# Kernel optimization log

Measured on AMD Instinct MI355X. Metric: run time of the kernel, lower is better.

The kernel has to match this reference:

```python
import jax, jax.numpy as jnp
import numpy as np

EPS = 1e-10

def norm_t(x, axis):
    # zero-mean + L2 normalize along `axis` (standard NCC normalization)
    xc = x - jnp.mean(x, axis=axis, keepdims=True)
    return xc / (jnp.linalg.norm(xc, axis=axis, keepdims=True) + EPS)

def setup_inputs() -> dict:
    key = jax.random.key(0)
    k1, k2 = jax.random.split(key)
    input_compressed = jax.random.normal(k1, (1, 16, 131072), dtype=jnp.float32)  # [B, K, N]
    cmat = jax.random.normal(k2, (16, 1024), dtype=jnp.float32)                   # [K, D]
    return {"input_compressed": input_compressed, "cmat": cmat}

def reference(input_compressed, cmat):
    a = norm_t(input_compressed, axis=-2)          # [B, K, N], normalized over K
    b = norm_t(cmat, axis=0)                       # [K, D],    normalized over K
    ncc = jnp.einsum('bkn,kd->bnd', a, b)          # [B, N, D] correlation volume
    # torch: argmax(transpose(ncc,-2,-1), dim=-2) -> argmax over D -> [B, N]
    pred_depths = jnp.argmax(ncc, axis=-1)         # [B, N] int depth-bin indices
    return pred_depths
```

## Files before the change

kernel.cpp:

```cpp
#include <hip/hip_runtime.h>
#include <hip/hip_bf16.h>
#include <math.h>

#define N_PTS  131072
#define K_DIM  16
#define D_BINS 1024
#define MARGIN_P 6e-4f

typedef short bf16x8 __attribute__((ext_vector_type(8)));
typedef float f32x4  __attribute__((ext_vector_type(4)));

#define WS_OFF_BN  64
#define WS_OFF_B1  65600
#define WS_OFF_B2  98368
#define WS_OFF_Z   131136
#define WS_OFF_WL  131152
#define WS_NEED    655440

__device__ __forceinline__ void norm_np(const float* __restrict__ p,
                                        int stride, int n, float* __restrict__ a) {
#pragma clang fp contract(off)
    float v[K_DIM];
#pragma unroll
    for (int k = 0; k < K_DIM; ++k) v[k] = p[(size_t)k * stride + n];
    float s = v[0];
#pragma unroll
    for (int k = 1; k < K_DIM; ++k) s = s + v[k];
    const float mean = s / 16.0f;
    float sq[K_DIM];
#pragma unroll
    for (int k = 0; k < K_DIM; ++k) { a[k] = v[k] - mean; sq[k] = a[k] * a[k]; }
    float ss = sq[0];
#pragma unroll
    for (int k = 1; k < K_DIM; ++k) ss = ss + sq[k];
    const float denom = sqrtf(ss) + 1e-10f;
#pragma unroll
    for (int k = 0; k < K_DIM; ++k) a[k] = a[k] / denom;
}

__device__ __forceinline__ unsigned short bf16_bits(float f) {
    __hip_bfloat16 h = __float2bfloat16(f);
    unsigned short u;
    __builtin_memcpy(&u, &h, 2);
    return u;
}
__device__ __forceinline__ float bf16_val(float f) {
    return __bfloat162float(__float2bfloat16(f));
}

__global__ __launch_bounds__(256) void prep_b(
    const float* __restrict__ cmat, float* __restrict__ bnT,
    unsigned short* __restrict__ B1, unsigned short* __restrict__ B2,
    unsigned short* __restrict__ zblk, int* __restrict__ wl_count) {
#pragma clang fp contract(off)
    if (blockIdx.x == 0) {
        if (threadIdx.x == 0) *wl_count = 0;
        if (threadIdx.x < 8) zblk[threadIdx.x] = 0;
    }
    const int d = blockIdx.x * 256 + threadIdx.x;
    if (d >= D_BINS) return;

    float t[K_DIM];
    norm_np(cmat, D_BINS, d, t);

    const int tile = d >> 4, n = d & 15;
#pragma unroll
    for (int k = 0; k < K_DIM; ++k) {
        bnT[d * K_DIM + k] = t[k];
        const float hi_f = bf16_val(t[k]);
        const int idx = tile * 256 + ((k >> 3) * 16 + n) * 8 + (k & 7);
        B1[idx] = bf16_bits(t[k]);
        B2[idx] = bf16_bits(t[k] - hi_f);
    }
}

__global__ __launch_bounds__(512, 8) void mfma_screen(
    const float* __restrict__ x, const uint4* __restrict__ B1,
    const uint4* __restrict__ B2,
    int* __restrict__ out, int* __restrict__ wl, int* __restrict__ wl_count) {
#pragma clang fp contract(off)
    __shared__ uint4 ldsB[2048];

    {
#pragma unroll
        for (int j = 0; j < 4; ++j)
            ldsB[threadIdx.x + j * 512] = B1[threadIdx.x + j * 512];
    }

    const int lane = threadIdx.x & 63;
    const int wv   = threadIdx.x >> 6;
    const int W    = blockIdx.x * 8 + wv;
    const int P    = W * 16;
    const int m    = lane & 15;
    const int q    = lane >> 4;

    bf16x8 A;
    {
        float a[K_DIM];
        norm_np(x, N_PTS, P + m, a);
        unsigned short els[8];
#pragma unroll
        for (int j = 0; j < 8; ++j) {
            const int k = (q & 1) * 8 + j;
            if (q < 2) els[j] = bf16_bits(a[k]);
            else       els[j] = bf16_bits(a[k] - bf16_val(a[k]));
        }
        __builtin_memcpy(&A, els, 16);
    }

    __syncthreads();

    const uint4* b1p = ldsB + (lane & 31);
    const int b2base = (lane < 32) ? lane : 2048;
    const int b2step = (lane < 32) ? 32 : 0;

    unsigned ub1[4], ub2[4];
#pragma unroll
    for (int r = 0; r < 4; ++r) { ub1[r] = 0u; ub2[r] = 0u; }

    const unsigned mask  = 0xFFFFF800u;
    const unsigned dbase = 2047u - (unsigned)m;

#pragma unroll 4
    for (int i = 0; i < 64; ++i) {
        const uint4 w1 = b1p[i * 32];
        const uint4 w2 = B2[b2base + i * b2step];
        const bf16x8 bf1 = __builtin_bit_cast(bf16x8, w1);
        const bf16x8 bf2 = __builtin_bit_cast(bf16x8, w2);

        f32x4 acc = __builtin_amdgcn_mfma_f32_16x16x32_bf16(
            A, bf1, (f32x4){2.f, 2.f, 2.f, 2.f}, 0, 0, 0);
        acc = __builtin_amdgcn_mfma_f32_16x16x32_bf16(A, bf2, acc, 0, 0, 0);

        const unsigned dcomp = dbase - (unsigned)(i * 16);
#pragma unroll
        for (int r = 0; r < 4; ++r) {
            const unsigned u = (__float_as_uint(acc[r]) & mask) | dcomp;
            const unsigned nx = max(ub1[r], u);
            ub2[r] = max(ub2[r], min(ub1[r], u));
            ub1[r] = nx;
        }
    }

#pragma unroll
    for (int r = 0; r < 4; ++r) {
        unsigned u1 = ub1[r], u2 = ub2[r];
#pragma unroll
        for (int s = 1; s <= 8; s <<= 1) {
            const unsigned o1 = (unsigned)__shfl_xor((int)u1, s, 16);
            const unsigned o2 = (unsigned)__shfl_xor((int)u2, s, 16);
            const unsigned n1 = max(u1, o1);
            u2 = max(min(u1, o1), max(u2, o2));
            u1 = n1;
        }
        if (m == 0) {
            const int p  = P + q * 4 + r;
            const float s1 = __uint_as_float(u1 & mask);
            const float s2 = __uint_as_float(u2 & mask);
            if (s1 - s2 > MARGIN_P) {
                out[p] = 2047 - (int)(u1 & 2047u);
            } else {
                const int pos = atomicAdd(wl_count, 1);
                wl[pos] = p;
            }
        }
    }
}

__global__ __launch_bounds__(256) void ncc_exact_refine(
    const float* __restrict__ x, const float* __restrict__ bnT,
    int* __restrict__ out, const int* __restrict__ wl,
    const int* __restrict__ wl_count) {
#pragma clang fp contract(off)
    const int count  = *wl_count;
    const int lane   = threadIdx.x & 63;
    const int wave   = (blockIdx.x * 256 + threadIdx.x) >> 6;
    const int nwaves = (gridDim.x * 256) >> 6;

    for (int i = wave; i < count; i += nwaves) {
        const int n = wl[i];
        float a[K_DIM];
        norm_np(x, N_PTS, n, a);

        float best = -3.402823466e38f;
        int   idx  = 0x7fffffff;
        const float4* b4 = (const float4*)bnT;
        for (int t = 0; t < 16; ++t) {
            const int d = t * 64 + lane;
            const float4 q0 = b4[d * 4 + 0];
            const float4 q1 = b4[d * 4 + 1];
            const float4 q2 = b4[d * 4 + 2];
            const float4 q3 = b4[d * 4 + 3];
            float sc;
            sc = a[0] * q0.x;
            sc = sc + a[1]  * q0.y; sc = sc + a[2]  * q0.z; sc = sc + a[3]  * q0.w;
            sc = sc + a[4]  * q1.x; sc = sc + a[5]  * q1.y; sc = sc + a[6]  * q1.z;
            sc = sc + a[7]  * q1.w; sc = sc + a[8]  * q2.x; sc = sc + a[9]  * q2.y;
            sc = sc + a[10] * q2.z; sc = sc + a[11] * q2.w; sc = sc + a[12] * q3.x;
            sc = sc + a[13] * q3.y; sc = sc + a[14] * q3.z; sc = sc + a[15] * q3.w;
            if (sc > best) { best = sc; idx = d; }
        }
#pragma unroll
        for (int mk = 1; mk <= 32; mk <<= 1) {
            const float ob = __shfl_xor(best, mk);
            const int   oi = __shfl_xor(idx,  mk);
            if (ob > best || (ob == best && oi < idx)) { best = ob; idx = oi; }
        }
        if (lane == 0) out[n] = idx;
    }
}

__global__ __launch_bounds__(256) void ncc_argmax_np32(
    const float* __restrict__ x, const float* __restrict__ bnT,
    int* __restrict__ out) {
#pragma clang fp contract(off)
    const int n = blockIdx.x * 256 + threadIdx.x;
    float a[K_DIM];
    norm_np(x, N_PTS, n, a);

    float best = -3.402823466e38f;
    int   idx  = 0;
    const float4* b4 = (const float4*)bnT;
#pragma unroll 2
    for (int d = 0; d < D_BINS; ++d) {
        const float4 q0 = b4[d * 4 + 0];
        const float4 q1 = b4[d * 4 + 1];
        const float4 q2 = b4[d * 4 + 2];
        const float4 q3 = b4[d * 4 + 3];
        float sc;
        sc = a[0] * q0.x;
        sc = sc + a[1]  * q0.y; sc = sc + a[2]  * q0.z; sc = sc + a[3]  * q0.w;
        sc = sc + a[4]  * q1.x; sc = sc + a[5]  * q1.y; sc = sc + a[6]  * q1.z;
        sc = sc + a[7]  * q1.w; sc = sc + a[8]  * q2.x; sc = sc + a[9]  * q2.y;
        sc = sc + a[10] * q2.z; sc = sc + a[11] * q2.w; sc = sc + a[12] * q3.x;
        sc = sc + a[13] * q3.y; sc = sc + a[14] * q3.z; sc = sc + a[15] * q3.w;
        if (sc > best) { best = sc; idx = d; }
    }
    out[n] = idx;
}

__global__ __launch_bounds__(256) void normalize_rows_only(
    const float* __restrict__ cmat, float* __restrict__ bnT) {
#pragma clang fp contract(off)
    const int d = blockIdx.x * 256 + threadIdx.x;
    if (d >= D_BINS) return;
    float t[K_DIM];
    norm_np(cmat, D_BINS, d, t);
#pragma unroll
    for (int k = 0; k < K_DIM; ++k) bnT[d * K_DIM + k] = t[k];
}

extern "C" void kernel_launch(void* const* d_in, const int* in_sizes, int n_in,
                              void* d_out, int out_size, void* d_ws, size_t ws_size,
                              hipStream_t stream) {
    const float* x    = (const float*)d_in[0];
    const float* cmat = (const float*)d_in[1];
    int* out = (int*)d_out;
    char* ws = (char*)d_ws;

    if (ws_size >= (size_t)WS_NEED) {
        int*            wl_count = (int*)ws;
        float*          bnT      = (float*)(ws + WS_OFF_BN);
        unsigned short* B1       = (unsigned short*)(ws + WS_OFF_B1);
        unsigned short* B2       = (unsigned short*)(ws + WS_OFF_B2);
        unsigned short* zblk     = (unsigned short*)(ws + WS_OFF_Z);
        int*            wl       = (int*)(ws + WS_OFF_WL);

        prep_b<<<4, 256, 0, stream>>>(cmat, bnT, B1, B2, zblk, wl_count);
        mfma_screen<<<1024, 512, 0, stream>>>(
            x, (const uint4*)(ws + WS_OFF_B1), (const uint4*)(ws + WS_OFF_B2),
            out, wl, wl_count);
        ncc_exact_refine<<<512, 256, 0, stream>>>(x, bnT, out, wl, wl_count);
    } else {
        float* bnT = (float*)(ws + WS_OFF_BN);
        normalize_rows_only<<<4, 256, 0, stream>>>(cmat, bnT);
        ncc_argmax_np32<<<512, 256, 0, stream>>>(x, bnT, out);
    }
}
```

Before: 106.9 us.

## Screen with single fp16 MFMA instead of split-bf16 pair, widen margin

Replaces the two-pass split-bf16 screening (hi and lo parts of A and B) with a single fp16 MFMA per tile. The B-low array and its global reads are dropped, and the A-low half is zeroed. The candidate margin is raised to cover the larger fp16 error, and the exact refine kernel gets twice as many blocks. This halves MFMA and global B traffic in the screening loop, but the wider margin may send more points to the exact refine pass.

```diff
diff --git a/kernel.cpp b/kernel.cpp
--- a/kernel.cpp
+++ b/kernel.cpp
@@ -1,21 +1,19 @@
 #include <hip/hip_runtime.h>
-#include <hip/hip_bf16.h>
+#include <hip/hip_fp16.h>
 #include <math.h>
 
 #define N_PTS  131072
 #define K_DIM  16
 #define D_BINS 1024
-#define MARGIN_P 6e-4f
-
-typedef short bf16x8 __attribute__((ext_vector_type(8)));
-typedef float f32x4  __attribute__((ext_vector_type(4)));
+#define MARGIN_P 3.2e-3f
+
+typedef _Float16 f16x8 __attribute__((ext_vector_type(8)));
+typedef float    f32x4 __attribute__((ext_vector_type(4)));
 
 #define WS_OFF_BN  64
-#define WS_OFF_B1  65600
-#define WS_OFF_B2  98368
-#define WS_OFF_Z   131136
-#define WS_OFF_WL  131152
-#define WS_NEED    655440
+#define WS_OFF_BH  65600
+#define WS_OFF_WL  98368
+#define WS_NEED    (WS_OFF_WL + 4 * N_PTS)
 
 __device__ __forceinline__ void norm_np(const float* __restrict__ p,
                                         int stride, int n, float* __restrict__ a) {
@@ -38,25 +36,16 @@
     for (int k = 0; k < K_DIM; ++k) a[k] = a[k] / denom;
 }
 
-__device__ __forceinline__ unsigned short bf16_bits(float f) {
-    __hip_bfloat16 h = __float2bfloat16(f);
-    unsigned short u;
-    __builtin_memcpy(&u, &h, 2);
-    return u;
-}
-__device__ __forceinline__ float bf16_val(float f) {
-    return __bfloat162float(__float2bfloat16(f));
+__device__ __forceinline__ unsigned short f16_bits(float f) {
+    const _Float16 h = (_Float16)f;
+    return __builtin_bit_cast(unsigned short, h);
 }
 
 __global__ __launch_bounds__(256) void prep_b(
     const float* __restrict__ cmat, float* __restrict__ bnT,
-    unsigned short* __restrict__ B1, unsigned short* __restrict__ B2,
-    unsigned short* __restrict__ zblk, int* __restrict__ wl_count) {
-#pragma clang fp contract(off)
-    if (blockIdx.x == 0) {
-        if (threadIdx.x == 0) *wl_count = 0;
-        if (threadIdx.x < 8) zblk[threadIdx.x] = 0;
-    }
+    unsigned short* __restrict__ Bh, int* __restrict__ wl_count) {
+#pragma clang fp contract(off)
+    if (blockIdx.x == 0 && threadIdx.x == 0) *wl_count = 0;
     const int d = blockIdx.x * 256 + threadIdx.x;
     if (d >= D_BINS) return;
 
@@ -67,16 +56,13 @@
 #pragma unroll
     for (int k = 0; k < K_DIM; ++k) {
         bnT[d * K_DIM + k] = t[k];
-        const float hi_f = bf16_val(t[k]);
         const int idx = tile * 256 + ((k >> 3) * 16 + n) * 8 + (k & 7);
-        B1[idx] = bf16_bits(t[k]);
-        B2[idx] = bf16_bits(t[k] - hi_f);
+        Bh[idx] = f16_bits(t[k]);
     }
 }
 
 __global__ __launch_bounds__(512, 8) void mfma_screen(
-    const float* __restrict__ x, const uint4* __restrict__ B1,
-    const uint4* __restrict__ B2,
+    const float* __restrict__ x, const uint4* __restrict__ Bh,
     int* __restrict__ out, int* __restrict__ wl, int* __restrict__ wl_count) {
 #pragma clang fp contract(off)
     __shared__ uint4 ldsB[2048];
@@ -84,7 +70,7 @@
     {
 #pragma unroll
         for (int j = 0; j < 4; ++j)
-            ldsB[threadIdx.x + j * 512] = B1[threadIdx.x + j * 512];
+            ldsB[threadIdx.x + j * 512] = Bh[threadIdx.x + j * 512];
     }
 
     const int lane = threadIdx.x & 63;
@@ -94,7 +80,7 @@
     const int m    = lane & 15;
     const int q    = lane >> 4;
 
-    bf16x8 A;
+    f16x8 A;
     {
         float a[K_DIM];
         norm_np(x, N_PTS, P + m, a);
@@ -102,17 +88,14 @@
 #pragma unroll
         for (int j = 0; j < 8; ++j) {
             const int k = (q & 1) * 8 + j;
-            if (q < 2) els[j] = bf16_bits(a[k]);
-            else       els[j] = bf16_bits(a[k] - bf16_val(a[k]));
+            els[j] = (q < 2) ? f16_bits(a[k]) : (unsigned short)0;
         }
         __builtin_memcpy(&A, els, 16);
     }
 
     __syncthreads();
 
-    const uint4* b1p = ldsB + (lane & 31);
-    const int b2base = (lane < 32) ? lane : 2048;
-    const int b2step = (lane < 32) ? 32 : 0;
+    const uint4* bp = ldsB + (lane & 31);
 
     unsigned ub1[4], ub2[4];
 #pragma unroll
@@ -123,14 +106,11 @@
 
 #pragma unroll 4
     for (int i = 0; i < 64; ++i) {
-        const uint4 w1 = b1p[i * 32];
-        const uint4 w2 = B2[b2base + i * b2step];
-        const bf16x8 bf1 = __builtin_bit_cast(bf16x8, w1);
-        const bf16x8 bf2 = __builtin_bit_cast(bf16x8, w2);
-
-        f32x4 acc = __builtin_amdgcn_mfma_f32_16x16x32_bf16(
-            A, bf1, (f32x4){2.f, 2.f, 2.f, 2.f}, 0, 0, 0);
-        acc = __builtin_amdgcn_mfma_f32_16x16x32_bf16(A, bf2, acc, 0, 0, 0);
+        const uint4 w1 = bp[i * 32];
+        const f16x8 bf = __builtin_bit_cast(f16x8, w1);
+
+        const f32x4 acc = __builtin_amdgcn_mfma_f32_16x16x32_f16(
+            A, bf, (f32x4){2.f, 2.f, 2.f, 2.f}, 0, 0, 0);
 
         const unsigned dcomp = dbase - (unsigned)(i * 16);
 #pragma unroll
@@ -261,16 +241,13 @@
     if (ws_size >= (size_t)WS_NEED) {
         int*            wl_count = (int*)ws;
         float*          bnT      = (float*)(ws + WS_OFF_BN);
-        unsigned short* B1       = (unsigned short*)(ws + WS_OFF_B1);
-        unsigned short* B2       = (unsigned short*)(ws + WS_OFF_B2);
-        unsigned short* zblk     = (unsigned short*)(ws + WS_OFF_Z);
+        unsigned short* Bh       = (unsigned short*)(ws + WS_OFF_BH);
         int*            wl       = (int*)(ws + WS_OFF_WL);
 
-        prep_b<<<4, 256, 0, stream>>>(cmat, bnT, B1, B2, zblk, wl_count);
+        prep_b<<<4, 256, 0, stream>>>(cmat, bnT, Bh, wl_count);
         mfma_screen<<<1024, 512, 0, stream>>>(
-            x, (const uint4*)(ws + WS_OFF_B1), (const uint4*)(ws + WS_OFF_B2),
-            out, wl, wl_count);
-        ncc_exact_refine<<<512, 256, 0, stream>>>(x, bnT, out, wl, wl_count);
+            x, (const uint4*)(ws + WS_OFF_BH), out, wl, wl_count);
+        ncc_exact_refine<<<1024, 256, 0, stream>>>(x, bnT, out, wl, wl_count);
     } else {
         float* bnT = (float*)(ws + WS_OFF_BN);
         normalize_rows_only<<<4, 256, 0, stream>>>(cmat, bnT);
```

After: 185.6 us. 73.6% more time.

## Replace global worklist atomic with per-block LDS worklists and per-block refine

Applied to the files above, without the earlier changes.

Ambiguous points no longer go through a single global atomic counter. Each screen block collects up to 64 of them in shared memory and writes a per-block count and list. The refine kernel now launches one block per screen block and processes that block's list, falling back to refining all 128 points when the list overflows. This removes global atomic contention and the serialized worklist, at the cost of an extra __syncthreads and possible load imbalance across refine blocks.

```diff
diff --git a/kernel.cpp b/kernel.cpp
--- a/kernel.cpp
+++ b/kernel.cpp
@@ -10,12 +10,13 @@
 typedef short bf16x8 __attribute__((ext_vector_type(8)));
 typedef float f32x4  __attribute__((ext_vector_type(4)));
 
-#define WS_OFF_BN  64
-#define WS_OFF_B1  65600
-#define WS_OFF_B2  98368
-#define WS_OFF_Z   131136
-#define WS_OFF_WL  131152
-#define WS_NEED    655440
+#define WS_OFF_CNT 0
+#define WS_OFF_BN  4096
+#define WS_OFF_B1  69632
+#define WS_OFF_B2  102400
+#define WS_OFF_Z   135168
+#define WS_OFF_WL  135184
+#define WS_NEED    397328
 
 __device__ __forceinline__ void norm_np(const float* __restrict__ p,
                                         int stride, int n, float* __restrict__ a) {
@@ -51,12 +52,9 @@
 __global__ __launch_bounds__(256) void prep_b(
     const float* __restrict__ cmat, float* __restrict__ bnT,
     unsigned short* __restrict__ B1, unsigned short* __restrict__ B2,
-    unsigned short* __restrict__ zblk, int* __restrict__ wl_count) {
-#pragma clang fp contract(off)
-    if (blockIdx.x == 0) {
-        if (threadIdx.x == 0) *wl_count = 0;
-        if (threadIdx.x < 8) zblk[threadIdx.x] = 0;
-    }
+    unsigned short* __restrict__ zblk) {
+#pragma clang fp contract(off)
+    if (blockIdx.x == 0 && threadIdx.x < 8) zblk[threadIdx.x] = 0;
     const int d = blockIdx.x * 256 + threadIdx.x;
     if (d >= D_BINS) return;
 
@@ -77,10 +75,13 @@
 __global__ __launch_bounds__(512, 8) void mfma_screen(
     const float* __restrict__ x, const uint4* __restrict__ B1,
     const uint4* __restrict__ B2,
-    int* __restrict__ out, int* __restrict__ wl, int* __restrict__ wl_count) {
+    int* __restrict__ out, int* __restrict__ wl, int* __restrict__ counts) {
 #pragma clang fp contract(off)
     __shared__ uint4 ldsB[2048];
-
+    __shared__ int s_cnt;
+    __shared__ int s_list[64];
+
+    if (threadIdx.x == 0) s_cnt = 0;
     {
 #pragma unroll
         for (int j = 0; j < 4; ++j)
@@ -160,53 +161,69 @@
             if (s1 - s2 > MARGIN_P) {
                 out[p] = 2047 - (int)(u1 & 2047u);
             } else {
-                const int pos = atomicAdd(wl_count, 1);
-                wl[pos] = p;
+                const int pos = atomicAdd(&s_cnt, 1);
+                if (pos < 64) s_list[pos] = p;
             }
         }
     }
+
+    __syncthreads();
+    const int c = s_cnt;
+    if (threadIdx.x == 0) counts[blockIdx.x] = c;
+    if ((int)threadIdx.x < (c < 64 ? c : 64))
+        wl[blockIdx.x * 64 + threadIdx.x] = s_list[threadIdx.x];
+}
+
+__device__ __forceinline__ void refine_point(
+    const float* __restrict__ x, const float* __restrict__ bnT,
+    int* __restrict__ out, int n, int lane) {
+#pragma clang fp contract(off)
+    float a[K_DIM];
+    norm_np(x, N_PTS, n, a);
+
+    float best = -3.402823466e38f;
+    int   idx  = 0x7fffffff;
+    const float4* b4 = (const float4*)bnT;
+    for (int t = 0; t < 16; ++t) {
+        const int d = t * 64 + lane;
+        const float4 q0 = b4[d * 4 + 0];
+        const float4 q1 = b4[d * 4 + 1];
+        const float4 q2 = b4[d * 4 + 2];
+        const float4 q3 = b4[d * 4 + 3];
+        float sc;
+        sc = a[0] * q0.x;
+        sc = sc + a[1]  * q0.y; sc = sc + a[2]  * q0.z; sc = sc + a[3]  * q0.w;
+        sc = sc + a[4]  * q1.x; sc = sc + a[5]  * q1.y; sc = sc + a[6]  * q1.z;
+        sc = sc + a[7]  * q1.w; sc = sc + a[8]  * q2.x; sc = sc + a[9]  * q2.y;
+        sc = sc + a[10] * q2.z; sc = sc + a[11] * q2.w; sc = sc + a[12] * q3.x;
+        sc = sc + a[13] * q3.y; sc = sc + a[14] * q3.z; sc = sc + a[15] * q3.w;
+        if (sc > best) { best = sc; idx = d; }
+    }
+#pragma unroll
+    for (int mk = 1; mk <= 32; mk <<= 1) {
+        const float ob = __shfl_xor(best, mk);
+        const int   oi = __shfl_xor(idx,  mk);
+        if (ob > best || (ob == best && oi < idx)) { best = ob; idx = oi; }
+    }
+    if (lane == 0) out[n] = idx;
 }
 
 __global__ __launch_bounds__(256) void ncc_exact_refine(
     const float* __restrict__ x, const float* __restrict__ bnT,
     int* __restrict__ out, const int* __restrict__ wl,
-    const int* __restrict__ wl_count) {
-#pragma clang fp contract(off)
-    const int count  = *wl_count;
-    const int lane   = threadIdx.x & 63;
-    const int wave   = (blockIdx.x * 256 + threadIdx.x) >> 6;
-    const int nwaves = (gridDim.x * 256) >> 6;
-
-    for (int i = wave; i < count; i += nwaves) {
-        const int n = wl[i];
-        float a[K_DIM];
-        norm_np(x, N_PTS, n, a);
-
-        float best = -3.402823466e38f;
-        int   idx  = 0x7fffffff;
-        const float4* b4 = (const float4*)bnT;
-        for (int t = 0; t < 16; ++t) {
-            const int d = t * 64 + lane;
-            const float4 q0 = b4[d * 4 + 0];
-            const float4 q1 = b4[d * 4 + 1];
-            const float4 q2 = b4[d * 4 + 2];
-            const float4 q3 = b4[d * 4 + 3];
-            float sc;
-            sc = a[0] * q0.x;
-            sc = sc + a[1]  * q0.y; sc = sc + a[2]  * q0.z; sc = sc + a[3]  * q0.w;
-            sc = sc + a[4]  * q1.x; sc = sc + a[5]  * q1.y; sc = sc + a[6]  * q1.z;
-            sc = sc + a[7]  * q1.w; sc = sc + a[8]  * q2.x; sc = sc + a[9]  * q2.y;
-            sc = sc + a[10] * q2.z; sc = sc + a[11] * q2.w; sc = sc + a[12] * q3.x;
-            sc = sc + a[13] * q3.y; sc = sc + a[14] * q3.z; sc = sc + a[15] * q3.w;
-            if (sc > best) { best = sc; idx = d; }
-        }
-#pragma unroll
-        for (int mk = 1; mk <= 32; mk <<= 1) {
-            const float ob = __shfl_xor(best, mk);
-            const int   oi = __shfl_xor(idx,  mk);
-            if (ob > best || (ob == best && oi < idx)) { best = ob; idx = oi; }
-        }
-        if (lane == 0) out[n] = idx;
+    const int* __restrict__ counts) {
+#pragma clang fp contract(off)
+    const int b    = blockIdx.x;
+    const int lane = threadIdx.x & 63;
+    const int wv   = threadIdx.x >> 6;
+    const int c    = counts[b];
+
+    if (c > 64) {
+        for (int i = wv; i < 128; i += 4)
+            refine_point(x, bnT, out, b * 128 + i, lane);
+    } else {
+        for (int i = wv; i < c; i += 4)
+            refine_point(x, bnT, out, wl[b * 64 + i], lane);
     }
 }
 
@@ -259,18 +276,18 @@
     char* ws = (char*)d_ws;
 
     if (ws_size >= (size_t)WS_NEED) {
-        int*            wl_count = (int*)ws;
-        float*          bnT      = (float*)(ws + WS_OFF_BN);
-        unsigned short* B1       = (unsigned short*)(ws + WS_OFF_B1);
-        unsigned short* B2       = (unsigned short*)(ws + WS_OFF_B2);
-        unsigned short* zblk     = (unsigned short*)(ws + WS_OFF_Z);
-        int*            wl       = (int*)(ws + WS_OFF_WL);
-
-        prep_b<<<4, 256, 0, stream>>>(cmat, bnT, B1, B2, zblk, wl_count);
+        int*            counts = (int*)(ws + WS_OFF_CNT);
+        float*          bnT    = (float*)(ws + WS_OFF_BN);
+        unsigned short* B1     = (unsigned short*)(ws + WS_OFF_B1);
+        unsigned short* B2     = (unsigned short*)(ws + WS_OFF_B2);
+        unsigned short* zblk   = (unsigned short*)(ws + WS_OFF_Z);
+        int*            wl     = (int*)(ws + WS_OFF_WL);
+
+        prep_b<<<4, 256, 0, stream>>>(cmat, bnT, B1, B2, zblk);
         mfma_screen<<<1024, 512, 0, stream>>>(
             x, (const uint4*)(ws + WS_OFF_B1), (const uint4*)(ws + WS_OFF_B2),
-            out, wl, wl_count);
-        ncc_exact_refine<<<512, 256, 0, stream>>>(x, bnT, out, wl, wl_count);
+            out, wl, counts);
+        ncc_exact_refine<<<1024, 256, 0, stream>>>(x, bnT, out, wl, counts);
     } else {
         float* bnT = (float*)(ws + WS_OFF_BN);
         normalize_rows_only<<<4, 256, 0, stream>>>(cmat, bnT);
```

Measured after the change: 114.1 us. 1.07x slower.

## Switch screening to 32x32x16 MFMA with split-bf16 hi/lo A operands

Applied to the files above, without the earlier changes.

Moves the screening GEMM from the 16x16x32 MFMA, where half the K dimension held low-order A parts, to the 32x32x16 MFMA. Each wave now handles 32 points, and the hi*hi, lo*hi and hi*lo products are issued as three separate MFMAs. The B matrix layout is reordered for the 32-wide tiles, the block size drops to 256 threads, and the per-lane top-2 tracking grows to 16 accumulators. This is meant to cut MFMA count and LDS traffic per point, at the cost of higher register pressure and fewer waves per block.

```diff
diff --git a/kernel.cpp b/kernel.cpp
--- a/kernel.cpp
+++ b/kernel.cpp
@@ -7,15 +7,14 @@
 #define D_BINS 1024
 #define MARGIN_P 6e-4f
 
-typedef short bf16x8 __attribute__((ext_vector_type(8)));
-typedef float f32x4  __attribute__((ext_vector_type(4)));
+typedef short bf16x8  __attribute__((ext_vector_type(8)));
+typedef float f32x16  __attribute__((ext_vector_type(16)));
 
 #define WS_OFF_BN  64
 #define WS_OFF_B1  65600
 #define WS_OFF_B2  98368
-#define WS_OFF_Z   131136
-#define WS_OFF_WL  131152
-#define WS_NEED    655440
+#define WS_OFF_WL  131136
+#define WS_NEED    655424
 
 __device__ __forceinline__ void norm_np(const float* __restrict__ p,
                                         int stride, int n, float* __restrict__ a) {
@@ -51,30 +50,28 @@
 __global__ __launch_bounds__(256) void prep_b(
     const float* __restrict__ cmat, float* __restrict__ bnT,
     unsigned short* __restrict__ B1, unsigned short* __restrict__ B2,
-    unsigned short* __restrict__ zblk, int* __restrict__ wl_count) {
-#pragma clang fp contract(off)
-    if (blockIdx.x == 0) {
-        if (threadIdx.x == 0) *wl_count = 0;
-        if (threadIdx.x < 8) zblk[threadIdx.x] = 0;
-    }
+    int* __restrict__ wl_count) {
+#pragma clang fp contract(off)
+    if (blockIdx.x == 0 && threadIdx.x == 0) *wl_count = 0;
     const int d = blockIdx.x * 256 + threadIdx.x;
     if (d >= D_BINS) return;
 
     float t[K_DIM];
     norm_np(cmat, D_BINS, d, t);
 
-    const int tile = d >> 4, n = d & 15;
+    const int tile = d >> 5, col = d & 31;
 #pragma unroll
     for (int k = 0; k < K_DIM; ++k) {
         bnT[d * K_DIM + k] = t[k];
-        const float hi_f = bf16_val(t[k]);
-        const int idx = tile * 256 + ((k >> 3) * 16 + n) * 8 + (k & 7);
+        const int lane = col + 32 * (k >> 3);
+        const int idx  = tile * 512 + lane * 8 + (k & 7);
+        const float hi = bf16_val(t[k]);
         B1[idx] = bf16_bits(t[k]);
-        B2[idx] = bf16_bits(t[k] - hi_f);
-    }
-}
-
-__global__ __launch_bounds__(512, 8) void mfma_screen(
+        B2[idx] = bf16_bits(t[k] - hi);
+    }
+}
+
+__global__ __launch_bounds__(256, 4) void mfma_screen(
     const float* __restrict__ x, const uint4* __restrict__ B1,
     const uint4* __restrict__ B2,
     int* __restrict__ out, int* __restrict__ wl, int* __restrict__ wl_count) {
@@ -83,58 +80,57 @@
 
     {
 #pragma unroll
-        for (int j = 0; j < 4; ++j)
-            ldsB[threadIdx.x + j * 512] = B1[threadIdx.x + j * 512];
+        for (int j = 0; j < 8; ++j)
+            ldsB[threadIdx.x + j * 256] = B1[threadIdx.x + j * 256];
     }
 
     const int lane = threadIdx.x & 63;
     const int wv   = threadIdx.x >> 6;
-    const int W    = blockIdx.x * 8 + wv;
-    const int P    = W * 16;
-    const int m    = lane & 15;
-    const int q    = lane >> 4;
-
-    bf16x8 A;
+    const int P    = (blockIdx.x * 4 + wv) * 32;
+    const int col  = lane & 31;
+    const int half = lane >> 5;
+
+    bf16x8 Ahi, Alo;
     {
         float a[K_DIM];
-        norm_np(x, N_PTS, P + m, a);
-        unsigned short els[8];
+        norm_np(x, N_PTS, P + col, a);
+        unsigned short eh[8], el[8];
 #pragma unroll
         for (int j = 0; j < 8; ++j) {
-            const int k = (q & 1) * 8 + j;
-            if (q < 2) els[j] = bf16_bits(a[k]);
-            else       els[j] = bf16_bits(a[k] - bf16_val(a[k]));
-        }
-        __builtin_memcpy(&A, els, 16);
+            const int k = half * 8 + j;
+            const float hi = bf16_val(a[k]);
+            eh[j] = bf16_bits(a[k]);
+            el[j] = bf16_bits(a[k] - hi);
+        }
+        __builtin_memcpy(&Ahi, eh, 16);
+        __builtin_memcpy(&Alo, el, 16);
     }
 
     __syncthreads();
 
-    const uint4* b1p = ldsB + (lane & 31);
-    const int b2base = (lane < 32) ? lane : 2048;
-    const int b2step = (lane < 32) ? 32 : 0;
-
-    unsigned ub1[4], ub2[4];
-#pragma unroll
-    for (int r = 0; r < 4; ++r) { ub1[r] = 0u; ub2[r] = 0u; }
+    unsigned ub1[16], ub2[16];
+#pragma unroll
+    for (int r = 0; r < 16; ++r) { ub1[r] = 0u; ub2[r] = 0u; }
 
     const unsigned mask  = 0xFFFFF800u;
-    const unsigned dbase = 2047u - (unsigned)m;
-
-#pragma unroll 4
-    for (int i = 0; i < 64; ++i) {
-        const uint4 w1 = b1p[i * 32];
-        const uint4 w2 = B2[b2base + i * b2step];
-        const bf16x8 bf1 = __builtin_bit_cast(bf16x8, w1);
-        const bf16x8 bf2 = __builtin_bit_cast(bf16x8, w2);
-
-        f32x4 acc = __builtin_amdgcn_mfma_f32_16x16x32_bf16(
-            A, bf1, (f32x4){2.f, 2.f, 2.f, 2.f}, 0, 0, 0);
-        acc = __builtin_amdgcn_mfma_f32_16x16x32_bf16(A, bf2, acc, 0, 0, 0);
-
-        const unsigned dcomp = dbase - (unsigned)(i * 16);
-#pragma unroll
-        for (int r = 0; r < 4; ++r) {
+    const unsigned dbase = 2047u - (unsigned)col;
+
+    f32x16 cinit;
+#pragma unroll
+    for (int r = 0; r < 16; ++r) cinit[r] = 2.0f;
+
+#pragma unroll 2
+    for (int i = 0; i < 32; ++i) {
+        const bf16x8 bh = __builtin_bit_cast(bf16x8, ldsB[i * 64 + lane]);
+        const bf16x8 bl = __builtin_bit_cast(bf16x8, B2[i * 64 + lane]);
+
+        f32x16 acc = __builtin_amdgcn_mfma_f32_32x32x16_bf16(Ahi, bh, cinit, 0, 0, 0);
+        acc = __builtin_amdgcn_mfma_f32_32x32x16_bf16(Alo, bh, acc, 0, 0, 0);
+        acc = __builtin_amdgcn_mfma_f32_32x32x16_bf16(Ahi, bl, acc, 0, 0, 0);
+
+        const unsigned dcomp = dbase - (unsigned)(i * 32);
+#pragma unroll
+        for (int r = 0; r < 16; ++r) {
             const unsigned u = (__float_as_uint(acc[r]) & mask) | dcomp;
             const unsigned nx = max(ub1[r], u);
             ub2[r] = max(ub2[r], min(ub1[r], u));
@@ -143,18 +139,19 @@
     }
 
 #pragma unroll
-    for (int r = 0; r < 4; ++r) {
+    for (int r = 0; r < 16; ++r) {
         unsigned u1 = ub1[r], u2 = ub2[r];
 #pragma unroll
-        for (int s = 1; s <= 8; s <<= 1) {
-            const unsigned o1 = (unsigned)__shfl_xor((int)u1, s, 16);
-            const unsigned o2 = (unsigned)__shfl_xor((int)u2, s, 16);
+        for (int s = 1; s <= 16; s <<= 1) {
+            const unsigned o1 = (unsigned)__shfl_xor((int)u1, s, 32);
+            const unsigned o2 = (unsigned)__shfl_xor((int)u2, s, 32);
             const unsigned n1 = max(u1, o1);
             u2 = max(min(u1, o1), max(u2, o2));
             u1 = n1;
         }
-        if (m == 0) {
-            const int p  = P + q * 4 + r;
+        if (col == 0) {
+            const int row = (r & 3) + 8 * (r >> 2) + 4 * half;
+            const int p   = P + row;
             const float s1 = __uint_as_float(u1 & mask);
             const float s2 = __uint_as_float(u2 & mask);
             if (s1 - s2 > MARGIN_P) {
@@ -263,11 +260,10 @@
         float*          bnT      = (float*)(ws + WS_OFF_BN);
         unsigned short* B1       = (unsigned short*)(ws + WS_OFF_B1);
         unsigned short* B2       = (unsigned short*)(ws + WS_OFF_B2);
-        unsigned short* zblk     = (unsigned short*)(ws + WS_OFF_Z);
         int*            wl       = (int*)(ws + WS_OFF_WL);
 
-        prep_b<<<4, 256, 0, stream>>>(cmat, bnT, B1, B2, zblk, wl_count);
-        mfma_screen<<<1024, 512, 0, stream>>>(
+        prep_b<<<4, 256, 0, stream>>>(cmat, bnT, B1, B2, wl_count);
+        mfma_screen<<<1024, 256, 0, stream>>>(
             x, (const uint4*)(ws + WS_OFF_B1), (const uint4*)(ws + WS_OFF_B2),
             out, wl, wl_count);
         ncc_exact_refine<<<512, 256, 0, stream>>>(x, bnT, out, wl, wl_count);
```

Result: slower. 109.3 us (+2.2%).
